# Kernel tuning notes

Measured on AMD Instinct MI355X. Metric: run time of the kernel, lower is better.

## Reference

```python
import jax, jax.numpy as jnp
import numpy as np

# RCGANConfig constants
D_X, D_EPS = 64, 16
A_VOCAB, A_EMB = 100, 32
T_VOCAB, T_EMB = 4, 16
D_H = 128
D_IN = A_EMB + T_EMB + D_X + D_EPS + 1  # 129 (use_prev_y adds 1)


def setup_inputs() -> dict:
    key = jax.random.key(0)
    ks = jax.random.split(key, 20)
    B, T = 1024, 256
    s = 0.05
    x = jax.random.normal(ks[0], (B, D_X), jnp.float32)
    a = jax.random.randint(ks[1], (B, T), 0, A_VOCAB, jnp.int32)
    t = jax.random.randint(ks[2], (B, T), 0, T_VOCAB, jnp.int32)
    y = (jax.random.uniform(ks[3], (B, T)) < 0.5).astype(jnp.float32)
    mask = jnp.ones((B, T), jnp.float32)
    eps = jax.random.normal(ks[4], (B, T, D_EPS), jnp.float32)
    # parameters
    Wx = jax.random.normal(ks[5], (D_X, D_X), jnp.float32) * s
    bx = jnp.zeros((D_X,), jnp.float32)
    Ea = jax.random.normal(ks[6], (A_VOCAB, A_EMB), jnp.float32) * s
    Et = jax.random.normal(ks[7], (T_VOCAB, T_EMB), jnp.float32) * s
    Wih = jax.random.normal(ks[8], (3 * D_H, D_IN), jnp.float32) * s
    Whh = jax.random.normal(ks[9], (3 * D_H, D_H), jnp.float32) * s
    bih = jnp.zeros((3 * D_H,), jnp.float32)
    bhh = jnp.zeros((3 * D_H,), jnp.float32)
    W0 = jax.random.normal(ks[10], (D_H, D_X + D_EPS), jnp.float32) * s
    b0 = jnp.zeros((D_H,), jnp.float32)
    Wy = jax.random.normal(ks[11], (1, D_H), jnp.float32) * s
    by = jnp.zeros((1,), jnp.float32)
    return {"x": x, "a": a, "t": t, "y": y, "mask": mask, "eps": eps,
            "Wx": Wx, "bx": bx, "Ea": Ea, "Et": Et, "Wih": Wih, "Whh": Whh,
            "bih": bih, "bhh": bhh, "W0": W0, "b0": b0, "Wy": Wy, "by": by}


def reference(x, a, t, y, mask, eps, Wx, bx, Ea, Et, Wih, Whh, bih, bhh, W0, b0, Wy, by):
    # teacher_forcing path, rnn='gru', use_prev_y=True, y provided, stochastic_y=False
    B, T = a.shape
    x_enc = x @ Wx.T + bx                                        # [B, d_x] (constant per step)
    h0 = jnp.tanh(jnp.concatenate([x_enc, eps[:, 0, :]], -1) @ W0.T + b0)  # [B, d_h]
    # prev_y: zeros at t=0, then detached teacher signal y[:, t-1]
    prev_y = jnp.concatenate(
        [jnp.zeros((B, 1), y.dtype), jax.lax.stop_gradient(y[:, :-1])], axis=1)[..., None]  # [B,T,1]
    a_enc = Ea[a]                                                # [B,T,a_emb]
    t_enc = Et[t]                                                # [B,T,t_emb]
    inp = jnp.concatenate(
        [a_enc, t_enc, jnp.broadcast_to(x_enc[:, None, :], (B, T, x_enc.shape[-1])), eps, prev_y],
        axis=-1)                                                 # [B,T,d_in]
    gates_x = inp @ Wih.T + bih                                  # [B,T,3*d_h] precomputed input gates

    def step(h, gx):
        gh = h @ Whh.T + bhh
        gx_r, gx_z, gx_n = jnp.split(gx, 3, axis=-1)
        gh_r, gh_z, gh_n = jnp.split(gh, 3, axis=-1)
        r = jax.nn.sigmoid(gx_r + gh_r)
        z = jax.nn.sigmoid(gx_z + gh_z)
        n = jnp.tanh(gx_n + r * gh_n)
        h_new = (1.0 - z) * n + z * h
        return h_new, h_new

    _, hs = jax.lax.scan(step, h0, jnp.swapaxes(gates_x, 0, 1))  # hs: [T,B,d_h]
    hs = jnp.swapaxes(hs, 0, 1)                                  # [B,T,d_h]
    logits = hs @ Wy.T + by                                      # [B,T,1]
    prob = jax.nn.sigmoid(logits)
    m = mask[..., None]
    logits_o = m * logits + (1.0 - m) * jax.lax.stop_gradient(logits)
    y_o = m * prob + (1.0 - m) * jax.lax.stop_gradient(prob)
    # stacked: [..., 0] = y_logits, [..., 1] = y
    return jnp.concatenate([logits_o, y_o], axis=-1)             # [B,T,2]
```

## Files before the change

kernel.cpp:

```cpp
#include <hip/hip_runtime.h>
#include <hip/hip_bf16.h>

typedef __attribute__((ext_vector_type(8))) short bfrag;
typedef __attribute__((ext_vector_type(4))) float ffrag;

#define NB 1024
#define NT 256

static __device__ __forceinline__ float fast_rcp(float x) { return __builtin_amdgcn_rcpf(x); }
static __device__ __forceinline__ float sigm(float x) {
  return fast_rcp(1.f + __builtin_amdgcn_exp2f(-1.44269504f * x));
}
static __device__ __forceinline__ float tanh_f(float x) {
  return __builtin_fmaf(2.f, fast_rcp(1.f + __builtin_amdgcn_exp2f(-2.88539008f * x)), -1.f);
}
static __device__ __forceinline__ float bf2f(__hip_bfloat16 v) { return __bfloat162float(v); }
static __device__ __forceinline__ short f2bs(float f) {
  __hip_bfloat16 h = __float2bfloat16(f);
  return *reinterpret_cast<short*>(&h);
}
static __device__ __forceinline__ void barrier_lgkm() {
  asm volatile("s_waitcnt lgkmcnt(0)\n\ts_barrier" ::: "memory");
}

__global__ __launch_bounds__(512, 2) void gru_kernel(
    const float* __restrict__ x,
    const int* __restrict__ a_ids,
    const int* __restrict__ t_ids,
    const float* __restrict__ y,
    const float* __restrict__ eps,
    const float* __restrict__ Wx,
    const float* __restrict__ bx,
    const float* __restrict__ Ea,
    const float* __restrict__ Et,
    const float* __restrict__ Wih,
    const float* __restrict__ Whh,
    const float* __restrict__ bih,
    const float* __restrict__ bhh,
    const float* __restrict__ W0,
    const float* __restrict__ b0g,
    const float* __restrict__ Wy,
    const float* __restrict__ by,
    float* __restrict__ out)
{
  __shared__ __align__(16) __hip_bfloat16 h_bf[2][16][136];
  __shared__ __align__(16) __hip_bfloat16 ind_s[2][16][72];
  __shared__ __align__(16) __hip_bfloat16 Ea_s[100][40];
  __shared__ __align__(16) __hip_bfloat16 Et_s[4][16];
  __shared__ float prevy_s[2][16];
  __shared__ float bsum_r[128], bsum_z[128], bihn_s[128], bhhn_s[128];
  __shared__ float wprev_s[384];
  __shared__ __align__(16) char uni[38912];
  unsigned short* aid_s   = (unsigned short*)(uni);
  unsigned short* tix_s   = (unsigned short*)(uni + 8192);
  __hip_bfloat16* eps_ch  = (__hip_bfloat16*)(uni + 16384);
  float*          y_ch    = (float*)(uni + 32768);
  float*          out_b   = (float*)(uni + 34816);
  __hip_bfloat16* Wxb     = (__hip_bfloat16*)(uni);
  __hip_bfloat16* W0b     = (__hip_bfloat16*)(uni + 8192);
  float*          x_s     = (float*)(uni + 28672);
  float*          eps0s   = (float*)(uni + 32832);
  float*          xe_s    = (float*)(uni + 33920);
  float*          h0f     = (float*)(uni);

  const int tid = threadIdx.x;
  const int w = tid >> 6, l = tid & 63;
  const int lmod = l & 15, ldiv = l >> 4;
  const int i_own = 16 * w + lmod;
  const int b0 = blockIdx.x * 16;

  if (tid < 128) {
    bsum_r[tid] = bih[tid] + bhh[tid];
    bsum_z[tid] = bih[128 + tid] + bhh[128 + tid];
    bihn_s[tid] = bih[256 + tid];
    bhhn_s[tid] = bhh[256 + tid];
  }
  if (tid < 384) wprev_s[tid] = Wih[tid * 129 + 128];
  for (int j = tid; j < 3200; j += 512) {
    int r = j >> 5, c = j & 31;
    Ea_s[r][c] = __float2bfloat16(Ea[j]);
  }
  if (tid < 64) ((__hip_bfloat16*)Et_s)[tid] = __float2bfloat16(Et[tid]);
  for (int j = tid; j < 4096; j += 512)  Wxb[j] = __float2bfloat16(Wx[j]);
  for (int j = tid; j < 10240; j += 512) W0b[j] = __float2bfloat16(W0[j]);
  for (int j = tid; j < 1024; j += 512) {
    int r = j >> 6, c = j & 63;
    x_s[r * 65 + c] = x[(b0 + r) * 64 + c];
  }
  if (tid < 256) {
    int r = tid >> 4, c = tid & 15;
    eps0s[r * 17 + c] = eps[((b0 + r) * NT) * 16 + c];
  }
  const float by_f = by[0];

  bfrag Bh[3][4], Bi[3][2];
  #pragma unroll
  for (int g = 0; g < 3; g++) {
    int n = (g * 8 + w) * 16 + lmod;
    #pragma unroll
    for (int kc = 0; kc < 4; kc++) {
      int k = kc * 32 + ldiv * 8;
      const float* wh = Whh + n * 128 + k;
      float4 h0v = *reinterpret_cast<const float4*>(wh);
      float4 h1v = *reinterpret_cast<const float4*>(wh + 4);
      bfrag th = {f2bs(h0v.x), f2bs(h0v.y), f2bs(h0v.z), f2bs(h0v.w),
                  f2bs(h1v.x), f2bs(h1v.y), f2bs(h1v.z), f2bs(h1v.w)};
      Bh[g][kc] = th;
    }
    #pragma unroll
    for (int kc = 0; kc < 2; kc++) {
      bfrag ti;
      #pragma unroll
      for (int j = 0; j < 8; j++) {
        int dk = kc * 32 + ldiv * 8 + j;
        int col = dk < 48 ? dk : dk + 64;
        ti[j] = f2bs(Wih[n * 129 + col]);
      }
      Bi[g][kc] = ti;
    }
  }
  bfrag Bl[4];
  if (w == 7) {
    #pragma unroll
    for (int kc = 0; kc < 4; kc++) {
      bfrag bt;
      #pragma unroll
      for (int j = 0; j < 8; j++)
        bt[j] = (lmod == 0) ? f2bs(Wy[kc * 32 + ldiv * 8 + j]) : (short)0;
      Bl[kc] = bt;
    }
  }
  __syncthreads();

  for (int j = tid; j < 1024; j += 512) {
    int r = j & 15, i = j >> 4;
    float acc = bx[i];
    #pragma unroll 8
    for (int k = 0; k < 64; k++) acc += x_s[r * 65 + k] * bf2f(Wxb[i * 64 + k]);
    xe_s[r * 65 + i] = acc;
    h_bf[1][r][i] = __float2bfloat16(acc);
  }
  __syncthreads();

  for (int j = tid; j < 2048; j += 512) {
    int r = j & 15, o = j >> 4;
    float acc = b0g[o];
    #pragma unroll 8
    for (int k = 0; k < 64; k++) acc += xe_s[r * 65 + k] * bf2f(W0b[o * 80 + k]);
    #pragma unroll
    for (int k = 0; k < 16; k++) acc += eps0s[r * 17 + k] * bf2f(W0b[o * 80 + 64 + k]);
    h0f[r * 128 + o] = tanh_f(acc);
  }

  ffrag gxc[3];
  {
    ffrag z = {0.f, 0.f, 0.f, 0.f};
    gxc[0] = z; gxc[1] = z; gxc[2] = z;
    #pragma unroll
    for (int kc = 0; kc < 2; kc++) {
      bfrag axd = *reinterpret_cast<const bfrag*>(&h_bf[1][lmod][kc * 32 + ldiv * 8]);
      #pragma unroll
      for (int g = 0; g < 3; g++) {
        int n = (g * 8 + w) * 16 + lmod;
        const float* wi = Wih + n * 129 + 48 + kc * 32 + ldiv * 8;
        bfrag bt;
        #pragma unroll
        for (int j = 0; j < 8; j++) bt[j] = f2bs(wi[j]);
        gxc[g] = __builtin_amdgcn_mfma_f32_16x16x32_bf16(axd, bt, gxc[g], 0, 0, 0);
      }
    }
    float brf = bsum_r[i_own], bzf = bsum_z[i_own], bn1 = bihn_s[i_own];
    #pragma unroll
    for (int q = 0; q < 4; q++) {
      gxc[0][q] += brf;
      gxc[1][q] += bzf;
      gxc[2][q] += bn1;
    }
  }
  __syncthreads();

  float h_reg[4];
  #pragma unroll
  for (int q = 0; q < 4; q++) {
    int row = ldiv * 4 + q;
    float hv = h0f[row * 128 + i_own];
    h_reg[q] = hv;
    h_bf[0][row][i_own] = __float2bfloat16(hv);
  }
  __syncthreads();

  for (int j = tid; j < 4096; j += 512) {
    int r = j >> 8, t = j & 255;
    aid_s[r * 256 + t] = (unsigned short)a_ids[(b0 + r) * NT + t];
    tix_s[r * 256 + t] = (unsigned short)t_ids[(b0 + r) * NT + t];
  }
  {
    int r = tid >> 5, sub = tid & 31;
    const float* p = eps + ((b0 + r) * NT + 0) * 16 + sub * 8;
    float4 eA = *reinterpret_cast<const float4*>(p);
    float4 eB = *reinterpret_cast<const float4*>(p + 4);
    int toff = sub >> 1, c8 = (sub & 1) * 8;
    bfrag e = {f2bs(eA.x), f2bs(eA.y), f2bs(eA.z), f2bs(eA.w),
               f2bs(eB.x), f2bs(eB.y), f2bs(eB.z), f2bs(eB.w)};
    *reinterpret_cast<bfrag*>(&eps_ch[(toff * 16 + r) * 16 + c8]) = e;
    if (tid < 64) {
      int r2 = tid >> 2, s2 = tid & 3;
      float4 yv = *reinterpret_cast<const float4*>(y + (b0 + r2) * NT + s2 * 4);
      *reinterpret_cast<float4*>(&y_ch[r2 * 16 + s2 * 4]) = yv;
    }
  }
  if (tid < 16) prevy_s[0][tid] = 0.f;
  __syncthreads();

  const bool do_emb = (tid >= 256 && tid < 384);
  const int er8 = (tid - 256) >> 3, ch = (tid - 256) & 7;
  if (do_emb) {
    int j = tid - 256, r = j >> 3, c = j & 7;
    bfrag e;
    if (c < 4)      e = *reinterpret_cast<const bfrag*>(&Ea_s[aid_s[r * 256]][c * 8]);
    else if (c < 6) e = *reinterpret_cast<const bfrag*>(&Et_s[tix_s[r * 256]][(c - 4) * 8]);
    else            e = *reinterpret_cast<const bfrag*>(&eps_ch[(r) * 16 + (c - 6) * 8]);
    *reinterpret_cast<bfrag*>(&ind_s[0][r][c * 8]) = e;
  }
  const float wpr = wprev_s[i_own], wpz = wprev_s[128 + i_own], wpn = wprev_s[256 + i_own];
  const float bn2 = bhhn_s[i_own];
  __syncthreads();

  for (int t = 0; t < NT; t++) {
    const int buf = t & 1, nbuf = buf ^ 1;

    if ((t & 15) == 1 && t > 16 && tid < 128) {
      int fc = (t - 17) >> 4;
      int r = tid >> 3, k = tid & 7;
      int s = fc * 16 + 2 * k, slot = s & 31;
      float4 v;
      v.x = out_b[slot * 32 + r * 2];
      v.y = out_b[slot * 32 + r * 2 + 1];
      v.z = out_b[(slot + 1) * 32 + r * 2];
      v.w = out_b[(slot + 1) * 32 + r * 2 + 1];
      *reinterpret_cast<float4*>(out + ((b0 + r) * NT + s) * 2) = v;
    }

    const bool ck = ((t & 15) == 0) && (t + 16 < NT);
    float4 eA, eB, yv;
    const int cr = tid >> 5, csub = tid & 31;
    if (ck) {
      const float* p = eps + ((b0 + cr) * NT + t + 16) * 16 + csub * 8;
      eA = *reinterpret_cast<const float4*>(p);
      eB = *reinterpret_cast<const float4*>(p + 4);
      if (tid < 64) {
        int r2 = tid >> 2, s2 = tid & 3;
        yv = *reinterpret_cast<const float4*>(y + (b0 + r2) * NT + t + 16 + s2 * 4);
      }
    }

    const int t1 = (t + 1 < NT) ? t + 1 : NT - 1;
    if (do_emb) {
      bfrag e;
      if (ch < 4)      e = *reinterpret_cast<const bfrag*>(&Ea_s[aid_s[er8 * 256 + t1]][ch * 8]);
      else if (ch < 6) e = *reinterpret_cast<const bfrag*>(&Et_s[tix_s[er8 * 256 + t1]][(ch - 4) * 8]);
      else             e = *reinterpret_cast<const bfrag*>(
                           &eps_ch[((((t1 >> 4) & 1) * 16 + (t1 & 15)) * 16 + er8) * 16 + (ch - 6) * 8]);
      *reinterpret_cast<bfrag*>(&ind_s[nbuf][er8][ch * 8]) = e;
    }
    if (tid >= 384 && tid < 400) {
      int r = tid - 384;
      prevy_s[nbuf][r] = y_ch[((t >> 4) & 1) * 256 + r * 16 + (t & 15)];
    }

    ffrag ar = gxc[0], az = gxc[1], anx = gxc[2], anh, agl;
    #pragma unroll
    for (int q = 0; q < 4; q++) anh[q] = bn2;
    #pragma unroll
    for (int kc = 0; kc < 2; kc++) {
      bfrag ax = *reinterpret_cast<const bfrag*>(&ind_s[buf][lmod][kc * 32 + ldiv * 8]);
      ar  = __builtin_amdgcn_mfma_f32_16x16x32_bf16(ax, Bi[0][kc], ar, 0, 0, 0);
      az  = __builtin_amdgcn_mfma_f32_16x16x32_bf16(ax, Bi[1][kc], az, 0, 0, 0);
      anx = __builtin_amdgcn_mfma_f32_16x16x32_bf16(ax, Bi[2][kc], anx, 0, 0, 0);
    }
    if (w == 7) {
      #pragma unroll
      for (int q = 0; q < 4; q++) agl[q] = by_f;
    }
    #pragma unroll
    for (int kc = 0; kc < 4; kc++) {
      bfrag ah = *reinterpret_cast<const bfrag*>(&h_bf[buf][lmod][kc * 32 + ldiv * 8]);
      ar  = __builtin_amdgcn_mfma_f32_16x16x32_bf16(ah, Bh[0][kc], ar, 0, 0, 0);
      az  = __builtin_amdgcn_mfma_f32_16x16x32_bf16(ah, Bh[1][kc], az, 0, 0, 0);
      anh = __builtin_amdgcn_mfma_f32_16x16x32_bf16(ah, Bh[2][kc], anh, 0, 0, 0);
      if (w == 7)
        agl = __builtin_amdgcn_mfma_f32_16x16x32_bf16(ah, Bl[kc], agl, 0, 0, 0);
    }

    if (w == 7 && t > 0 && lmod == 0) {
      int slot = (t - 1) & 31;
      #pragma unroll
      for (int q = 0; q < 4; q++) {
        int row = ldiv * 4 + q;
        float lg = agl[q];
        out_b[slot * 32 + row * 2]     = lg;
        out_b[slot * 32 + row * 2 + 1] = sigm(lg);
      }
    }

    #pragma unroll
    for (int q = 0; q < 4; q++) {
      int row = ldiv * 4 + q;
      float py = prevy_s[buf][row];
      float rv = sigm(__builtin_fmaf(py, wpr, ar[q]));
      float zv = sigm(__builtin_fmaf(py, wpz, az[q]));
      float nv = tanh_f(__builtin_fmaf(py, wpn, anx[q]) + rv * anh[q]);
      float hn = __builtin_fmaf(zv, h_reg[q] - nv, nv);
      h_reg[q] = hn;
      h_bf[nbuf][row][i_own] = __float2bfloat16(hn);
    }

    if (ck) {
      int cb = ((t >> 4) + 1) & 1;
      int toff = csub >> 1, c8 = (csub & 1) * 8;
      bfrag e = {f2bs(eA.x), f2bs(eA.y), f2bs(eA.z), f2bs(eA.w),
                 f2bs(eB.x), f2bs(eB.y), f2bs(eB.z), f2bs(eB.w)};
      *reinterpret_cast<bfrag*>(&eps_ch[((cb * 16 + toff) * 16 + cr) * 16 + c8]) = e;
      if (tid < 64) {
        int r2 = tid >> 2, s2 = tid & 3;
        *reinterpret_cast<float4*>(&y_ch[cb * 256 + r2 * 16 + s2 * 4]) = yv;
      }
    }

    barrier_lgkm();
  }

  if (w == 7) {
    ffrag agl;
    #pragma unroll
    for (int q = 0; q < 4; q++) agl[q] = by_f;
    #pragma unroll
    for (int kc = 0; kc < 4; kc++) {
      bfrag ah = *reinterpret_cast<const bfrag*>(&h_bf[0][lmod][kc * 32 + ldiv * 8]);
      agl = __builtin_amdgcn_mfma_f32_16x16x32_bf16(ah, Bl[kc], agl, 0, 0, 0);
    }
    if (lmod == 0) {
      #pragma unroll
      for (int q = 0; q < 4; q++) {
        int row = ldiv * 4 + q;
        float lg = agl[q];
        out_b[31 * 32 + row * 2]     = lg;
        out_b[31 * 32 + row * 2 + 1] = sigm(lg);
      }
    }
  }
  __syncthreads();
  if (tid < 128) {
    int r = tid >> 3, k = tid & 7;
    int s = 240 + 2 * k, slot = s & 31;
    float4 v;
    v.x = out_b[slot * 32 + r * 2];
    v.y = out_b[slot * 32 + r * 2 + 1];
    v.z = out_b[(slot + 1) * 32 + r * 2];
    v.w = out_b[(slot + 1) * 32 + r * 2 + 1];
    *reinterpret_cast<float4*>(out + ((b0 + r) * NT + s) * 2) = v;
  }
}

extern "C" void kernel_launch(void* const* d_in, const int* in_sizes, int n_in,
                              void* d_out, int out_size, void* d_ws, size_t ws_size,
                              hipStream_t stream) {
  const float* x   = (const float*)d_in[0];
  const int*   a   = (const int*)d_in[1];
  const int*   tt  = (const int*)d_in[2];
  const float* y   = (const float*)d_in[3];
  const float* eps = (const float*)d_in[5];
  const float* Wx  = (const float*)d_in[6];
  const float* bx  = (const float*)d_in[7];
  const float* Ea  = (const float*)d_in[8];
  const float* Et  = (const float*)d_in[9];
  const float* Wih = (const float*)d_in[10];
  const float* Whh = (const float*)d_in[11];
  const float* bih = (const float*)d_in[12];
  const float* bhh = (const float*)d_in[13];
  const float* W0  = (const float*)d_in[14];
  const float* b0  = (const float*)d_in[15];
  const float* Wy  = (const float*)d_in[16];
  const float* by  = (const float*)d_in[17];
  float* out = (float*)d_out;

  gru_kernel<<<NB / 16, 512, 0, stream>>>(x, a, tt, y, eps, Wx, bx, Ea, Et,
                                          Wih, Whh, bih, bhh, W0, b0, Wy, by, out);
}
```

Baseline: 368.0 us.

## Gather GRU input-gate operands directly and precompute next step's input MFMAs off the critical path

Drops the ind_s staging buffer. Each wave now reads its A-operands straight from the embedding tables and the eps chunk, using a packed (a_id | t_id<<8) index laid out per timestep. The input-gate MFMAs for step t+1 are issued after the h update of step t, so only the Whh MFMAs stay on the recurrent critical path. The sigmoid/tanh exponent scales are folded into the weights and biases so the activations skip a multiply. The eps chunk gets a padded stride, and the layout of uni is reorganized; the extra bf16 rounding of the scaled weights may change numerics slightly.

```diff
diff --git a/kernel.cpp b/kernel.cpp
--- a/kernel.cpp
+++ b/kernel.cpp
@@ -6,10 +6,19 @@
 
 #define NB 1024
 #define NT 256
+
+#define KSIG -1.44269504f
+#define KTAN -2.88539008f
 
 static __device__ __forceinline__ float fast_rcp(float x) { return __builtin_amdgcn_rcpf(x); }
 static __device__ __forceinline__ float sigm(float x) {
   return fast_rcp(1.f + __builtin_amdgcn_exp2f(-1.44269504f * x));
+}
+static __device__ __forceinline__ float sigm_pre(float s) {
+  return fast_rcp(1.f + __builtin_amdgcn_exp2f(s));
+}
+static __device__ __forceinline__ float tanh_pre(float s) {
+  return __builtin_fmaf(2.f, fast_rcp(1.f + __builtin_amdgcn_exp2f(s)), -1.f);
 }
 static __device__ __forceinline__ float tanh_f(float x) {
   return __builtin_fmaf(2.f, fast_rcp(1.f + __builtin_amdgcn_exp2f(-2.88539008f * x)), -1.f);
@@ -44,16 +53,14 @@
     float* __restrict__ out)
 {
   __shared__ __align__(16) __hip_bfloat16 h_bf[2][16][136];
-  __shared__ __align__(16) __hip_bfloat16 ind_s[2][16][72];
   __shared__ __align__(16) __hip_bfloat16 Ea_s[100][40];
   __shared__ __align__(16) __hip_bfloat16 Et_s[4][16];
   __shared__ float prevy_s[2][16];
   __shared__ float bsum_r[128], bsum_z[128], bihn_s[128], bhhn_s[128];
   __shared__ float wprev_s[384];
   __shared__ __align__(16) char uni[38912];
-  unsigned short* aid_s   = (unsigned short*)(uni);
-  unsigned short* tix_s   = (unsigned short*)(uni + 8192);
-  __hip_bfloat16* eps_ch  = (__hip_bfloat16*)(uni + 16384);
+  unsigned short* id_s    = (unsigned short*)(uni);
+  __hip_bfloat16* eps_ch  = (__hip_bfloat16*)(uni + 8192);
   float*          y_ch    = (float*)(uni + 32768);
   float*          out_b   = (float*)(uni + 34816);
   __hip_bfloat16* Wxb     = (__hip_bfloat16*)(uni);
@@ -70,12 +77,12 @@
   const int b0 = blockIdx.x * 16;
 
   if (tid < 128) {
-    bsum_r[tid] = bih[tid] + bhh[tid];
-    bsum_z[tid] = bih[128 + tid] + bhh[128 + tid];
-    bihn_s[tid] = bih[256 + tid];
-    bhhn_s[tid] = bhh[256 + tid];
-  }
-  if (tid < 384) wprev_s[tid] = Wih[tid * 129 + 128];
+    bsum_r[tid] = KSIG * (bih[tid] + bhh[tid]);
+    bsum_z[tid] = KSIG * (bih[128 + tid] + bhh[128 + tid]);
+    bihn_s[tid] = KTAN * bih[256 + tid];
+    bhhn_s[tid] = KTAN * bhh[256 + tid];
+  }
+  if (tid < 384) wprev_s[tid] = ((tid < 256) ? KSIG : KTAN) * Wih[tid * 129 + 128];
   for (int j = tid; j < 3200; j += 512) {
     int r = j >> 5, c = j & 31;
     Ea_s[r][c] = __float2bfloat16(Ea[j]);
@@ -96,6 +103,7 @@
   bfrag Bh[3][4], Bi[3][2];
   #pragma unroll
   for (int g = 0; g < 3; g++) {
+    const float sg = (g < 2) ? KSIG : KTAN;
     int n = (g * 8 + w) * 16 + lmod;
     #pragma unroll
     for (int kc = 0; kc < 4; kc++) {
@@ -103,8 +111,8 @@
       const float* wh = Whh + n * 128 + k;
       float4 h0v = *reinterpret_cast<const float4*>(wh);
       float4 h1v = *reinterpret_cast<const float4*>(wh + 4);
-      bfrag th = {f2bs(h0v.x), f2bs(h0v.y), f2bs(h0v.z), f2bs(h0v.w),
-                  f2bs(h1v.x), f2bs(h1v.y), f2bs(h1v.z), f2bs(h1v.w)};
+      bfrag th = {f2bs(sg * h0v.x), f2bs(sg * h0v.y), f2bs(sg * h0v.z), f2bs(sg * h0v.w),
+                  f2bs(sg * h1v.x), f2bs(sg * h1v.y), f2bs(sg * h1v.z), f2bs(sg * h1v.w)};
       Bh[g][kc] = th;
     }
     #pragma unroll
@@ -114,7 +122,7 @@
       for (int j = 0; j < 8; j++) {
         int dk = kc * 32 + ldiv * 8 + j;
         int col = dk < 48 ? dk : dk + 64;
-        ti[j] = f2bs(Wih[n * 129 + col]);
+        ti[j] = f2bs(sg * Wih[n * 129 + col]);
       }
       Bi[g][kc] = ti;
     }
@@ -161,11 +169,12 @@
       bfrag axd = *reinterpret_cast<const bfrag*>(&h_bf[1][lmod][kc * 32 + ldiv * 8]);
       #pragma unroll
       for (int g = 0; g < 3; g++) {
+        const float sg = (g < 2) ? KSIG : KTAN;
         int n = (g * 8 + w) * 16 + lmod;
         const float* wi = Wih + n * 129 + 48 + kc * 32 + ldiv * 8;
         bfrag bt;
         #pragma unroll
-        for (int j = 0; j < 8; j++) bt[j] = f2bs(wi[j]);
+        for (int j = 0; j < 8; j++) bt[j] = f2bs(sg * wi[j]);
         gxc[g] = __builtin_amdgcn_mfma_f32_16x16x32_bf16(axd, bt, gxc[g], 0, 0, 0);
       }
     }
@@ -191,18 +200,19 @@
 
   for (int j = tid; j < 4096; j += 512) {
     int r = j >> 8, t = j & 255;
-    aid_s[r * 256 + t] = (unsigned short)a_ids[(b0 + r) * NT + t];
-    tix_s[r * 256 + t] = (unsigned short)t_ids[(b0 + r) * NT + t];
+    unsigned short v = (unsigned short)(a_ids[(b0 + r) * NT + t] |
+                                        (t_ids[(b0 + r) * NT + t] << 8));
+    id_s[t * 16 + r] = v;
   }
   {
     int r = tid >> 5, sub = tid & 31;
-    const float* p = eps + ((b0 + r) * NT + 0) * 16 + sub * 8;
+    const float* p = eps + ((b0 + r) * NT) * 16 + sub * 8;
     float4 eA = *reinterpret_cast<const float4*>(p);
     float4 eB = *reinterpret_cast<const float4*>(p + 4);
     int toff = sub >> 1, c8 = (sub & 1) * 8;
     bfrag e = {f2bs(eA.x), f2bs(eA.y), f2bs(eA.z), f2bs(eA.w),
                f2bs(eB.x), f2bs(eB.y), f2bs(eB.z), f2bs(eB.w)};
-    *reinterpret_cast<bfrag*>(&eps_ch[(toff * 16 + r) * 16 + c8]) = e;
+    *reinterpret_cast<bfrag*>(&eps_ch[(toff * 16 + r) * 24 + c8]) = e;
     if (tid < 64) {
       int r2 = tid >> 2, s2 = tid & 3;
       float4 yv = *reinterpret_cast<const float4*>(y + (b0 + r2) * NT + s2 * 4);
@@ -210,21 +220,28 @@
     }
   }
   if (tid < 16) prevy_s[0][tid] = 0.f;
-  __syncthreads();
-
-  const bool do_emb = (tid >= 256 && tid < 384);
-  const int er8 = (tid - 256) >> 3, ch = (tid - 256) & 7;
-  if (do_emb) {
-    int j = tid - 256, r = j >> 3, c = j & 7;
-    bfrag e;
-    if (c < 4)      e = *reinterpret_cast<const bfrag*>(&Ea_s[aid_s[r * 256]][c * 8]);
-    else if (c < 6) e = *reinterpret_cast<const bfrag*>(&Et_s[tix_s[r * 256]][(c - 4) * 8]);
-    else            e = *reinterpret_cast<const bfrag*>(&eps_ch[(r) * 16 + (c - 6) * 8]);
-    *reinterpret_cast<bfrag*>(&ind_s[0][r][c * 8]) = e;
-  }
   const float wpr = wprev_s[i_own], wpz = wprev_s[128 + i_own], wpn = wprev_s[256 + i_own];
   const float bn2 = bhhn_s[i_own];
-  __syncthreads();
+  const char* const ea_base  = (const char*)Ea_s + ldiv * 16;
+  const char* const et_base  = (const char*)Et_s + ldiv * 16;
+  const char* const eps_base = (const char*)eps_ch + lmod * 48 + (ldiv - 2) * 16;
+  __syncthreads();
+
+  ffrag pa0 = gxc[0], pa1 = gxc[1], pa2 = gxc[2];
+  {
+    int id = id_s[lmod];
+    int aid = id & 127, tv = id >> 8;
+    bfrag axA = *reinterpret_cast<const bfrag*>(ea_base + aid * 80);
+    const char* etp = et_base + tv * 32;
+    const char* epp = eps_base;
+    bfrag axB = *reinterpret_cast<const bfrag*>(ldiv < 2 ? etp : epp);
+    pa0 = __builtin_amdgcn_mfma_f32_16x16x32_bf16(axA, Bi[0][0], pa0, 0, 0, 0);
+    pa1 = __builtin_amdgcn_mfma_f32_16x16x32_bf16(axA, Bi[1][0], pa1, 0, 0, 0);
+    pa2 = __builtin_amdgcn_mfma_f32_16x16x32_bf16(axA, Bi[2][0], pa2, 0, 0, 0);
+    pa0 = __builtin_amdgcn_mfma_f32_16x16x32_bf16(axB, Bi[0][1], pa0, 0, 0, 0);
+    pa1 = __builtin_amdgcn_mfma_f32_16x16x32_bf16(axB, Bi[1][1], pa1, 0, 0, 0);
+    pa2 = __builtin_amdgcn_mfma_f32_16x16x32_bf16(axB, Bi[2][1], pa2, 0, 0, 0);
+  }
 
   for (int t = 0; t < NT; t++) {
     const int buf = t & 1, nbuf = buf ^ 1;
@@ -254,42 +271,26 @@
       }
     }
 
-    const int t1 = (t + 1 < NT) ? t + 1 : NT - 1;
-    if (do_emb) {
-      bfrag e;
-      if (ch < 4)      e = *reinterpret_cast<const bfrag*>(&Ea_s[aid_s[er8 * 256 + t1]][ch * 8]);
-      else if (ch < 6) e = *reinterpret_cast<const bfrag*>(&Et_s[tix_s[er8 * 256 + t1]][(ch - 4) * 8]);
-      else             e = *reinterpret_cast<const bfrag*>(
-                           &eps_ch[((((t1 >> 4) & 1) * 16 + (t1 & 15)) * 16 + er8) * 16 + (ch - 6) * 8]);
-      *reinterpret_cast<bfrag*>(&ind_s[nbuf][er8][ch * 8]) = e;
-    }
+    ffrag anh, agl;
+    #pragma unroll
+    for (int q = 0; q < 4; q++) anh[q] = bn2;
+    if (w == 7) {
+      #pragma unroll
+      for (int q = 0; q < 4; q++) agl[q] = by_f;
+    }
+    #pragma unroll
+    for (int kc = 0; kc < 4; kc++) {
+      bfrag ah = *reinterpret_cast<const bfrag*>(&h_bf[buf][lmod][kc * 32 + ldiv * 8]);
+      pa0 = __builtin_amdgcn_mfma_f32_16x16x32_bf16(ah, Bh[0][kc], pa0, 0, 0, 0);
+      pa1 = __builtin_amdgcn_mfma_f32_16x16x32_bf16(ah, Bh[1][kc], pa1, 0, 0, 0);
+      anh = __builtin_amdgcn_mfma_f32_16x16x32_bf16(ah, Bh[2][kc], anh, 0, 0, 0);
+      if (w == 7)
+        agl = __builtin_amdgcn_mfma_f32_16x16x32_bf16(ah, Bl[kc], agl, 0, 0, 0);
+    }
+
     if (tid >= 384 && tid < 400) {
       int r = tid - 384;
       prevy_s[nbuf][r] = y_ch[((t >> 4) & 1) * 256 + r * 16 + (t & 15)];
-    }
-
-    ffrag ar = gxc[0], az = gxc[1], anx = gxc[2], anh, agl;
-    #pragma unroll
-    for (int q = 0; q < 4; q++) anh[q] = bn2;
-    #pragma unroll
-    for (int kc = 0; kc < 2; kc++) {
-      bfrag ax = *reinterpret_cast<const bfrag*>(&ind_s[buf][lmod][kc * 32 + ldiv * 8]);
-      ar  = __builtin_amdgcn_mfma_f32_16x16x32_bf16(ax, Bi[0][kc], ar, 0, 0, 0);
-      az  = __builtin_amdgcn_mfma_f32_16x16x32_bf16(ax, Bi[1][kc], az, 0, 0, 0);
-      anx = __builtin_amdgcn_mfma_f32_16x16x32_bf16(ax, Bi[2][kc], anx, 0, 0, 0);
-    }
-    if (w == 7) {
-      #pragma unroll
-      for (int q = 0; q < 4; q++) agl[q] = by_f;
-    }
-    #pragma unroll
-    for (int kc = 0; kc < 4; kc++) {
-      bfrag ah = *reinterpret_cast<const bfrag*>(&h_bf[buf][lmod][kc * 32 + ldiv * 8]);
-      ar  = __builtin_amdgcn_mfma_f32_16x16x32_bf16(ah, Bh[0][kc], ar, 0, 0, 0);
-      az  = __builtin_amdgcn_mfma_f32_16x16x32_bf16(ah, Bh[1][kc], az, 0, 0, 0);
-      anh = __builtin_amdgcn_mfma_f32_16x16x32_bf16(ah, Bh[2][kc], anh, 0, 0, 0);
-      if (w == 7)
-        agl = __builtin_amdgcn_mfma_f32_16x16x32_bf16(ah, Bl[kc], agl, 0, 0, 0);
     }
 
     if (w == 7 && t > 0 && lmod == 0) {
@@ -307,23 +308,41 @@
     for (int q = 0; q < 4; q++) {
       int row = ldiv * 4 + q;
       float py = prevy_s[buf][row];
-      float rv = sigm(__builtin_fmaf(py, wpr, ar[q]));
-      float zv = sigm(__builtin_fmaf(py, wpz, az[q]));
-      float nv = tanh_f(__builtin_fmaf(py, wpn, anx[q]) + rv * anh[q]);
+      float rv = sigm_pre(__builtin_fmaf(py, wpr, pa0[q]));
+      float zv = sigm_pre(__builtin_fmaf(py, wpz, pa1[q]));
+      float nv = tanh_pre(__builtin_fmaf(rv, anh[q], __builtin_fmaf(py, wpn, pa2[q])));
       float hn = __builtin_fmaf(zv, h_reg[q] - nv, nv);
       h_reg[q] = hn;
       h_bf[nbuf][row][i_own] = __float2bfloat16(hn);
     }
 
+    if (t + 1 < NT) {
+      const int tn = t + 1;
+      const int ebase = (((tn >> 4) & 1) * 16 + (tn & 15)) * 16;
+      int id = id_s[tn * 16 + lmod];
+      int aid = id & 127, tv = id >> 8;
+      bfrag axA = *reinterpret_cast<const bfrag*>(ea_base + aid * 80);
+      const char* etp = et_base + tv * 32;
+      const char* epp = eps_base + ebase * 48;
+      bfrag axB = *reinterpret_cast<const bfrag*>(ldiv < 2 ? etp : epp);
+      pa0 = gxc[0]; pa1 = gxc[1]; pa2 = gxc[2];
+      pa0 = __builtin_amdgcn_mfma_f32_16x16x32_bf16(axA, Bi[0][0], pa0, 0, 0, 0);
+      pa1 = __builtin_amdgcn_mfma_f32_16x16x32_bf16(axA, Bi[1][0], pa1, 0, 0, 0);
+      pa2 = __builtin_amdgcn_mfma_f32_16x16x32_bf16(axA, Bi[2][0], pa2, 0, 0, 0);
+      pa0 = __builtin_amdgcn_mfma_f32_16x16x32_bf16(axB, Bi[0][1], pa0, 0, 0, 0);
+      pa1 = __builtin_amdgcn_mfma_f32_16x16x32_bf16(axB, Bi[1][1], pa1, 0, 0, 0);
+      pa2 = __builtin_amdgcn_mfma_f32_16x16x32_bf16(axB, Bi[2][1], pa2, 0, 0, 0);
+    }
+
     if (ck) {
-      int cb = ((t >> 4) + 1) & 1;
+      int cb2 = ((t >> 4) + 1) & 1;
       int toff = csub >> 1, c8 = (csub & 1) * 8;
       bfrag e = {f2bs(eA.x), f2bs(eA.y), f2bs(eA.z), f2bs(eA.w),
                  f2bs(eB.x), f2bs(eB.y), f2bs(eB.z), f2bs(eB.w)};
-      *reinterpret_cast<bfrag*>(&eps_ch[((cb * 16 + toff) * 16 + cr) * 16 + c8]) = e;
+      *reinterpret_cast<bfrag*>(&eps_ch[((cb2 * 16 + toff) * 16 + cr) * 24 + c8]) = e;
       if (tid < 64) {
         int r2 = tid >> 2, s2 = tid & 3;
-        *reinterpret_cast<float4*>(&y_ch[cb * 256 + r2 * 16 + s2 * 4]) = yv;
+        *reinterpret_cast<float4*>(&y_ch[cb2 * 256 + r2 * 16 + s2 * 4]) = yv;
       }
     }
 
```

New measurement: 352.0 us. 1.05x faster.
